# Kernel tuning notes

Hardware: AMD Instinct MI355X
Metric: run time of the kernel (lower is better)

The kernel has to match this reference:

```python
import jax, jax.numpy as jnp
import numpy as np

EPS = 1e-10        # matches eps in calculate_jeffreys_similarity
NEG = -1e30        # finite 'masked out' logit (avoids NaN for absent classes)
NORM_EPS = 1e-12   # F.normalize clamp


def setup_inputs() -> dict:
    key = jax.random.key(0)
    k1, k2, k3 = jax.random.split(key, 3)
    B, D, H, W = 4, 256, 256, 256
    C, P = 16, 5
    feature_map = jax.random.normal(k1, (B, D, H, W), dtype=jnp.float32)
    prototypes = jax.random.normal(k2, (C * P, D), dtype=jnp.float32)
    gt_mask = jax.random.randint(k3, (B, H, W), 0, C, dtype=jnp.int32)
    return {
        "feature_map": feature_map,
        "prototypes": prototypes,
        "gt_mask": gt_mask,
        "num_prototypes_per_class": P,
    }


def _loss(feature_map, prototypes, gt_mask, P):
    B, D, H, W = feature_map.shape
    N = H * W
    C = prototypes.shape[0] // P

    # [B, N, D] L2-normalized pixel features (F.normalize, eps=1e-12)
    feats = feature_map.reshape(B, D, N).transpose(0, 2, 1)
    feats = feats / jnp.maximum(jnp.linalg.norm(feats, axis=-1, keepdims=True), NORM_EPS)

    # [C, P, D] L2-normalized prototypes
    protos = prototypes.reshape(C, P, D)
    protos = protos / jnp.maximum(jnp.linalg.norm(protos, axis=-1, keepdims=True), NORM_EPS)

    # per-class pixel membership mask [B, C, N]
    mask = gt_mask.reshape(B, 1, N) == jnp.arange(C, dtype=gt_mask.dtype)[None, :, None]
    present = jnp.any(mask, axis=-1)                        # [B, C]

    # cosine similarities: [B, C, P, N]
    sims = jnp.einsum('bnd,cpd->bcpn', feats, protos)

    m = mask[:, :, None, :]                                 # [B, C, 1, N]
    # first softmax over the pixels of the class (original: softmax(similarities, dim=0))
    s1 = jax.nn.softmax(jnp.where(m, sims, NEG), axis=-1)
    # second softmax applied inside calculate_jeffreys_similarity (over the same gathered pixels)
    s2 = jax.nn.softmax(jnp.where(m, s1, NEG), axis=-1)

    # V = distribution + eps; off-mask positions are exactly eps, and since
    # eps*(log eps - log eps)=0 they contribute nothing to the KL sums below,
    # so summing over all N reproduces the gathered-pixel sum exactly.
    V = jnp.where(m, s2, 0.0) + EPS                          # [B, C, P, N]
    logV = jnp.log(V)

    A = jnp.sum(V * logV, axis=-1)                           # [B, C, P]
    # Bmat[b,c,i,j] = sum_n logV[i] * V[j]
    Bmat = jnp.einsum('bcin,bcjn->bcij', logV, V)
    # KL(V_j || V_i) = A[j] - Bmat[i, j]
    M = A[:, :, None, :] - Bmat                              # [B, C, P, P]
    J = M + jnp.swapaxes(M, -1, -2)                          # Jeffreys divergence (symmetric)
    simmat = jnp.exp(-J)                                     # pairwise similarity

    P_ = simmat.shape[-1]
    triu = jnp.triu(jnp.ones((P_, P_), dtype=simmat.dtype), k=1)
    num_pairs = P_ * (P_ - 1) // 2
    class_sim = jnp.sum(simmat * triu, axis=(-1, -2)) / num_pairs   # [B, C]

    # mean over classes that actually appear in the image; empty image -> 0
    class_sim = jnp.where(present, class_sim, 0.0)
    cnt = jnp.sum(present, axis=-1).astype(class_sim.dtype)          # [B]
    batch_loss = jnp.where(cnt > 0, jnp.sum(class_sim, axis=-1) / jnp.maximum(cnt, 1.0), 0.0)
    return jnp.sum(batch_loss) / B


def reference(feature_map, prototypes, gt_mask, num_prototypes_per_class):
    return _loss(feature_map, prototypes, gt_mask, num_prototypes_per_class)
```

## Files before the change

kernel.cpp:

```cpp
#include <hip/hip_runtime.h>
#include <math.h>

#define BB 4
#define DD 256
#define NN 65536
#define CC 16
#define PP 5
#define CP 80
#define EPSV 1e-10f
#define PITCH 264

#define OFF_PLANE  20480
#define OFF_ACC    (OFF_PLANE + BB * PP * NN)
#define ACC_FLOATS (320 + 320 + 64 + BB * CC * 16)

__device__ __forceinline__ unsigned short f2bf(float f) {
    unsigned int u = __float_as_uint(f);
    u += 0x7fffu + ((u >> 16) & 1u);
    return (unsigned short)(u >> 16);
}

__global__ void k_norm(const float* __restrict__ protos,
                       float* __restrict__ protosN,
                       float* __restrict__ acc) {
    if (blockIdx.x == CP) {
        for (int i = threadIdx.x; i < ACC_FLOATS; i += 256) acc[i] = 0.f;
        return;
    }
    int r = blockIdx.x;
    int d = threadIdx.x;
    float v = protos[r * DD + d];
    __shared__ float red[256];
    red[d] = v * v;
    __syncthreads();
    for (int s = 128; s > 0; s >>= 1) {
        if (d < s) red[d] += red[d + s];
        __syncthreads();
    }
    float inv = 1.f / fmaxf(sqrtf(red[0]), 1e-12f);
    protosN[r * DD + d] = v * inv;
}

__device__ __forceinline__ void loadgv(const float* __restrict__ fb, int g,
                                       float4 (&f)[8]) {
    const float* p = fb + (size_t)g * 8 * NN;
    #pragma unroll
    for (int k = 0; k < 8; ++k)
        f[k] = *reinterpret_cast<const float4*>(p + (size_t)k * NN);
}

__device__ __forceinline__ void compv(const char* lb0, const char* lb1,
                                      const char* lb2, const char* lb3,
                                      const float4 (&f)[8], int g,
                                      float (&dot)[4][PP], float (&nrm)[4]) {
    const char* lbs[4] = {lb0, lb1, lb2, lb3};
    #pragma unroll
    for (int x = 0; x < 4; ++x) {
        uint4 q[PP];
        #pragma unroll
        for (int p = 0; p < PP; ++p)
            q[p] = *reinterpret_cast<const uint4*>(lbs[x] + p * (PITCH * 2) + g * 16);
        #pragma unroll
        for (int k = 0; k < 8; ++k) {
            float fx = (&f[k].x)[x];
            nrm[x] = fmaf(fx, fx, nrm[x]);
            #pragma unroll
            for (int p = 0; p < PP; ++p) {
                unsigned int w = (&q[p].x)[k >> 1];
                float a = __uint_as_float((k & 1) ? (w & 0xffff0000u) : (w << 16));
                dot[x][p] = fmaf(fx, a, dot[x][p]);
            }
        }
    }
}

__global__ __launch_bounds__(256) void k_sims(const float* __restrict__ fmap,
                                              const float* __restrict__ protosN,
                                              const int* __restrict__ gt,
                                              float* __restrict__ plane,
                                              float* __restrict__ denom1,
                                              float* __restrict__ cnt) {
    __shared__ __align__(16) unsigned short lp[CP * PITCH];
    __shared__ float bins[CP];
    __shared__ float binc[CC];
    const int tid = threadIdx.x;
    const int b   = blockIdx.x >> 6;
    const int n0  = ((blockIdx.x & 63) << 10) + (tid << 2);

    if (tid < CP) bins[tid] = 0.f;
    if (tid < CC) binc[tid] = 0.f;

    for (int idx = tid; idx < 5120; idx += 256) {
        int cp = idx >> 6, q = idx & 63;
        float4 v = *reinterpret_cast<const float4*>(&protosN[(cp << 8) + (q << 2)]);
        unsigned int u0 = (unsigned int)f2bf(v.x) | ((unsigned int)f2bf(v.y) << 16);
        unsigned int u1 = (unsigned int)f2bf(v.z) | ((unsigned int)f2bf(v.w) << 16);
        *reinterpret_cast<uint2*>(reinterpret_cast<char*>(lp) + cp * (PITCH * 2) + (q << 3))
            = make_uint2(u0, u1);
    }
    __syncthreads();

    const int4 cls = *reinterpret_cast<const int4*>(&gt[(size_t)b * NN + n0]);
    const char* lpc = reinterpret_cast<const char*>(lp);
    const char* lb0 = lpc + cls.x * (PP * PITCH * 2);
    const char* lb1 = lpc + cls.y * (PP * PITCH * 2);
    const char* lb2 = lpc + cls.z * (PP * PITCH * 2);
    const char* lb3 = lpc + cls.w * (PP * PITCH * 2);
    const float* fb = fmap + (size_t)b * DD * NN + n0;

    float dot[4][PP] = {{0.f,0.f,0.f,0.f,0.f},{0.f,0.f,0.f,0.f,0.f},
                        {0.f,0.f,0.f,0.f,0.f},{0.f,0.f,0.f,0.f,0.f}};
    float nrm[4] = {0.f, 0.f, 0.f, 0.f};
    float4 fA[8], fB[8];

    loadgv(fb, 0, fA);
    #pragma unroll 1
    for (int g = 0; g < 32; g += 2) {
        loadgv(fb, g + 1, fB);
        compv(lb0, lb1, lb2, lb3, fA, g, dot, nrm);
        if (g < 30) loadgv(fb, g + 2, fA);
        compv(lb0, lb1, lb2, lb3, fB, g + 1, dot, nrm);
    }

    float inv[4];
    #pragma unroll
    for (int x = 0; x < 4; ++x) inv[x] = 1.f / fmaxf(sqrtf(nrm[x]), 1e-12f);

    const int c4[4] = {cls.x, cls.y, cls.z, cls.w};
    #pragma unroll
    for (int p = 0; p < PP; ++p) {
        float4 e;
        e.x = __expf(dot[0][p] * inv[0] - 1.f);
        e.y = __expf(dot[1][p] * inv[1] - 1.f);
        e.z = __expf(dot[2][p] * inv[2] - 1.f);
        e.w = __expf(dot[3][p] * inv[3] - 1.f);
        *reinterpret_cast<float4*>(&plane[(size_t)(b * PP + p) * NN + n0]) = e;
        atomicAdd(&bins[c4[0] * PP + p], e.x);
        atomicAdd(&bins[c4[1] * PP + p], e.y);
        atomicAdd(&bins[c4[2] * PP + p], e.z);
        atomicAdd(&bins[c4[3] * PP + p], e.w);
    }
    #pragma unroll
    for (int x = 0; x < 4; ++x) atomicAdd(&binc[c4[x]], 1.f);
    __syncthreads();
    if (tid < CP) atomicAdd(&denom1[b * CP + tid], bins[tid]);
    if (tid < CC) atomicAdd(&cnt[b * CC + tid], binc[tid]);
}

__global__ __launch_bounds__(256) void k_denom2(const int* __restrict__ gt,
                                                const float* __restrict__ plane,
                                                const float* __restrict__ denom1,
                                                float* __restrict__ denom2) {
    __shared__ float inv1s[CP];
    __shared__ float bins[4][CP];
    const int tid = threadIdx.x;
    const int w   = tid >> 6;
    const int b   = blockIdx.x >> 6;
    const int n0  = ((blockIdx.x & 63) << 10) + (tid << 2);
    if (tid < CP) inv1s[tid] = 1.f / denom1[b * CP + tid];
    for (int i = tid; i < 4 * CP; i += 256) (&bins[0][0])[i] = 0.f;
    __syncthreads();
    const int4 cls = *reinterpret_cast<const int4*>(&gt[(size_t)b * NN + n0]);
    #pragma unroll
    for (int p = 0; p < PP; ++p) {
        size_t idx = (size_t)(b * PP + p) * NN + n0;
        float4 e = *reinterpret_cast<const float4*>(&plane[idx]);
        atomicAdd(&bins[w][cls.x * PP + p], __expf(e.x * inv1s[cls.x * PP + p] - 1.f));
        atomicAdd(&bins[w][cls.y * PP + p], __expf(e.y * inv1s[cls.y * PP + p] - 1.f));
        atomicAdd(&bins[w][cls.z * PP + p], __expf(e.z * inv1s[cls.z * PP + p] - 1.f));
        atomicAdd(&bins[w][cls.w * PP + p], __expf(e.w * inv1s[cls.w * PP + p] - 1.f));
    }
    __syncthreads();
    if (tid < CP)
        atomicAdd(&denom2[b * CP + tid],
                  bins[0][tid] + bins[1][tid] + bins[2][tid] + bins[3][tid]);
}

__global__ __launch_bounds__(256) void k_bmat(const int* __restrict__ gt,
                                              const float* __restrict__ plane,
                                              const float* __restrict__ denom1,
                                              const float* __restrict__ denom2,
                                              float* __restrict__ Bbins) {
    __shared__ float inv1s[CP];
    __shared__ float inv2s[CP];
    __shared__ float sb[4][CC * 16];
    const int tid = threadIdx.x;
    const int w   = tid >> 6;
    const int b   = blockIdx.x >> 6;
    const int n0  = ((blockIdx.x & 63) << 10) + (tid << 2);
    if (tid < CP) {
        inv1s[tid] = 1.f / denom1[b * CP + tid];
        inv2s[tid] = 1.f / denom2[b * CP + tid];
    }
    for (int i = tid; i < 4 * CC * 16; i += 256) (&sb[0][0])[i] = 0.f;
    __syncthreads();
    const int4 cls = *reinterpret_cast<const int4*>(&gt[(size_t)b * NN + n0]);
    const int c4[4] = {cls.x, cls.y, cls.z, cls.w};
    float V[4][PP], L[4][PP];
    #pragma unroll
    for (int p = 0; p < PP; ++p) {
        size_t idx = (size_t)(b * PP + p) * NN + n0;
        float4 e = *reinterpret_cast<const float4*>(&plane[idx]);
        V[0][p] = fmaf(__expf(e.x * inv1s[cls.x * PP + p] - 1.f), inv2s[cls.x * PP + p], EPSV);
        V[1][p] = fmaf(__expf(e.y * inv1s[cls.y * PP + p] - 1.f), inv2s[cls.y * PP + p], EPSV);
        V[2][p] = fmaf(__expf(e.z * inv1s[cls.z * PP + p] - 1.f), inv2s[cls.z * PP + p], EPSV);
        V[3][p] = fmaf(__expf(e.w * inv1s[cls.w * PP + p] - 1.f), inv2s[cls.w * PP + p], EPSV);
    }
    #pragma unroll
    for (int q = 0; q < 4; ++q)
        #pragma unroll
        for (int p = 0; p < PP; ++p) L[q][p] = __logf(V[q][p]);
    #pragma unroll
    for (int q = 0; q < 4; ++q) {
        float* base = &sb[w][c4[q] * 16];
        #pragma unroll
        for (int i = 0; i < PP; ++i) atomicAdd(&base[i], L[q][i] * V[q][i]);
        int slot = 5;
        #pragma unroll
        for (int i = 0; i < PP; ++i)
            #pragma unroll
            for (int j = i + 1; j < PP; ++j) {
                atomicAdd(&base[slot], fmaf(L[q][i], V[q][j], L[q][j] * V[q][i]));
                ++slot;
            }
    }
    __syncthreads();
    for (int i = tid; i < CC * 16; i += 256)
        atomicAdd(&Bbins[b * CC * 16 + i], sb[0][i] + sb[1][i] + sb[2][i] + sb[3][i]);
}

__global__ void k_final(const float* __restrict__ Bbins,
                        const float* __restrict__ cnt,
                        float* __restrict__ out) {
    __shared__ float cs[BB * CC];
    __shared__ float pr[BB * CC];
    const int t = threadIdx.x;
    if (t < BB * CC) {
        const float* bb = &Bbins[t * 16];
        float s = 0.f;
        int slot = 5;
        #pragma unroll
        for (int i = 0; i < PP; ++i)
            for (int j = i + 1; j < PP; ++j) {
                float J = bb[i] + bb[j] - bb[slot];
                ++slot;
                s += __expf(-J);
            }
        bool present = cnt[t] > 0.f;
        cs[t] = present ? s * 0.1f : 0.f;
        pr[t] = present ? 1.f : 0.f;
    }
    __syncthreads();
    if (t == 0) {
        float total = 0.f;
        for (int b = 0; b < BB; ++b) {
            float sc = 0.f, np = 0.f;
            for (int c = 0; c < CC; ++c) { sc += cs[b * CC + c]; np += pr[b * CC + c]; }
            total += (np > 0.f) ? sc / np : 0.f;
        }
        out[0] = total / (float)BB;
    }
}

extern "C" void kernel_launch(void* const* d_in, const int* in_sizes, int n_in,
                              void* d_out, int out_size, void* d_ws, size_t ws_size,
                              hipStream_t stream) {
    const float* fmap   = (const float*)d_in[0];
    const float* protos = (const float*)d_in[1];
    const int*   gt     = (const int*)d_in[2];
    float* ws      = (float*)d_ws;
    float* protosN = ws;
    float* plane   = ws + OFF_PLANE;
    float* acc     = ws + OFF_ACC;
    float* denom1  = acc;
    float* denom2  = acc + 320;
    float* cnt     = acc + 640;
    float* Bbins   = acc + 704;
    float* out     = (float*)d_out;

    k_norm  <<<CP + 1, 256, 0, stream>>>(protos, protosN, acc);
    k_sims  <<<256, 256, 0, stream>>>(fmap, protosN, gt, plane, denom1, cnt);
    k_denom2<<<256, 256, 0, stream>>>(gt, plane, denom1, denom2);
    k_bmat  <<<256, 256, 0, stream>>>(gt, plane, denom1, denom2, Bbins);
    k_final <<<1, 64, 0, stream>>>(Bbins, cnt, out);
}
```

Before: 96.41 us.

## Fuse all stages into one cooperative kernel with grid syncs, keep sims in registers

Replaces the five separate launches with one cooperative kernel that separates the prototype normalisation, similarity, two softmax denominators, the Bmat accumulation and the final reduction with grid.sync. Per-pixel exp values now stay in registers across phases, so the plane buffer is no longer written to and re-read from global memory twice. It also swizzles the block-to-tile mapping, staggers each block's starting D chunk to spread memory traffic, and pads the shared bins to a stride of 17. In exchange it adds four grid-wide barriers and needs all 256 blocks to be co-resident.

```diff
diff --git a/kernel.cpp b/kernel.cpp
--- a/kernel.cpp
+++ b/kernel.cpp
@@ -1,5 +1,8 @@
 #include <hip/hip_runtime.h>
+#include <hip/hip_cooperative_groups.h>
 #include <math.h>
+
+namespace cg = cooperative_groups;
 
 #define BB 4
 #define DD 256
@@ -10,9 +13,8 @@
 #define EPSV 1e-10f
 #define PITCH 264
 
-#define OFF_PLANE  20480
-#define OFF_ACC    (OFF_PLANE + BB * PP * NN)
-#define ACC_FLOATS (320 + 320 + 64 + BB * CC * 16)
+#define OFF_ACC    20480
+#define ACC_FLOATS 1728
 
 __device__ __forceinline__ unsigned short f2bf(float f) {
     unsigned int u = __float_as_uint(f);
@@ -20,30 +22,9 @@
     return (unsigned short)(u >> 16);
 }
 
-__global__ void k_norm(const float* __restrict__ protos,
-                       float* __restrict__ protosN,
-                       float* __restrict__ acc) {
-    if (blockIdx.x == CP) {
-        for (int i = threadIdx.x; i < ACC_FLOATS; i += 256) acc[i] = 0.f;
-        return;
-    }
-    int r = blockIdx.x;
-    int d = threadIdx.x;
-    float v = protos[r * DD + d];
-    __shared__ float red[256];
-    red[d] = v * v;
-    __syncthreads();
-    for (int s = 128; s > 0; s >>= 1) {
-        if (d < s) red[d] += red[d + s];
-        __syncthreads();
-    }
-    float inv = 1.f / fmaxf(sqrtf(red[0]), 1e-12f);
-    protosN[r * DD + d] = v * inv;
-}
-
-__device__ __forceinline__ void loadgv(const float* __restrict__ fb, int g,
+__device__ __forceinline__ void loadgv(const float* __restrict__ fb, int gi,
                                        float4 (&f)[8]) {
-    const float* p = fb + (size_t)g * 8 * NN;
+    const float* p = fb + (size_t)gi * 8 * NN;
     #pragma unroll
     for (int k = 0; k < 8; ++k)
         f[k] = *reinterpret_cast<const float4*>(p + (size_t)k * NN);
@@ -51,7 +32,7 @@
 
 __device__ __forceinline__ void compv(const char* lb0, const char* lb1,
                                       const char* lb2, const char* lb3,
-                                      const float4 (&f)[8], int g,
+                                      const float4 (&f)[8], int gi,
                                       float (&dot)[4][PP], float (&nrm)[4]) {
     const char* lbs[4] = {lb0, lb1, lb2, lb3};
     #pragma unroll
@@ -59,7 +40,7 @@
         uint4 q[PP];
         #pragma unroll
         for (int p = 0; p < PP; ++p)
-            q[p] = *reinterpret_cast<const uint4*>(lbs[x] + p * (PITCH * 2) + g * 16);
+            q[p] = *reinterpret_cast<const uint4*>(lbs[x] + p * (PITCH * 2) + gi * 16);
         #pragma unroll
         for (int k = 0; k < 8; ++k) {
             float fx = (&f[k].x)[x];
@@ -74,33 +55,60 @@
     }
 }
 
-__global__ __launch_bounds__(256) void k_sims(const float* __restrict__ fmap,
-                                              const float* __restrict__ protosN,
-                                              const int* __restrict__ gt,
-                                              float* __restrict__ plane,
-                                              float* __restrict__ denom1,
-                                              float* __restrict__ cnt) {
-    __shared__ __align__(16) unsigned short lp[CP * PITCH];
-    __shared__ float bins[CP];
-    __shared__ float binc[CC];
+__global__ __launch_bounds__(256) void k_fused(const float* __restrict__ fmap,
+                                               const float* __restrict__ protos,
+                                               const int* __restrict__ gt,
+                                               float* __restrict__ protosN,
+                                               float* __restrict__ acc,
+                                               float* __restrict__ out) {
+    cg::grid_group grid = cg::this_grid();
+    __shared__ __align__(16) char smem[42624];
     const int tid = threadIdx.x;
-    const int b   = blockIdx.x >> 6;
-    const int n0  = ((blockIdx.x & 63) << 10) + (tid << 2);
+    const int bid = blockIdx.x;
+
+    float* denom1 = acc;
+    float* denom2 = acc + 320;
+    float* cnt    = acc + 640;
+    float* Bbins  = acc + 704;
+
+    if (bid < CP) {
+        float* red = reinterpret_cast<float*>(smem);
+        float v = protos[bid * DD + tid];
+        red[tid] = v * v;
+        __syncthreads();
+        for (int s = 128; s > 0; s >>= 1) {
+            if (tid < s) red[tid] += red[tid + s];
+            __syncthreads();
+        }
+        float inv = 1.f / fmaxf(sqrtf(red[0]), 1e-12f);
+        protosN[bid * DD + tid] = v * inv;
+    } else if (bid == CP) {
+        for (int i = tid; i < ACC_FLOATS; i += 256) acc[i] = 0.f;
+    }
+    grid.sync();
+
+    const int swz  = ((bid & 7) << 5) + (bid >> 3);
+    const int b    = swz >> 6;
+    const int n0   = ((swz & 63) << 10) + (tid << 2);
+    const int dph  = (bid & 7) << 2;
+
+    unsigned short* lp = reinterpret_cast<unsigned short*>(smem);
+    float* bins = reinterpret_cast<float*>(smem + 42240);
+    float* binc = reinterpret_cast<float*>(smem + 42560);
 
     if (tid < CP) bins[tid] = 0.f;
     if (tid < CC) binc[tid] = 0.f;
-
     for (int idx = tid; idx < 5120; idx += 256) {
         int cp = idx >> 6, q = idx & 63;
         float4 v = *reinterpret_cast<const float4*>(&protosN[(cp << 8) + (q << 2)]);
         unsigned int u0 = (unsigned int)f2bf(v.x) | ((unsigned int)f2bf(v.y) << 16);
         unsigned int u1 = (unsigned int)f2bf(v.z) | ((unsigned int)f2bf(v.w) << 16);
-        *reinterpret_cast<uint2*>(reinterpret_cast<char*>(lp) + cp * (PITCH * 2) + (q << 3))
-            = make_uint2(u0, u1);
+        *reinterpret_cast<uint2*>(smem + cp * (PITCH * 2) + (q << 3)) = make_uint2(u0, u1);
     }
     __syncthreads();
 
     const int4 cls = *reinterpret_cast<const int4*>(&gt[(size_t)b * NN + n0]);
+    const int c4[4] = {cls.x, cls.y, cls.z, cls.w};
     const char* lpc = reinterpret_cast<const char*>(lp);
     const char* lb0 = lpc + cls.x * (PP * PITCH * 2);
     const char* lb1 = lpc + cls.y * (PP * PITCH * 2);
@@ -113,152 +121,133 @@
     float nrm[4] = {0.f, 0.f, 0.f, 0.f};
     float4 fA[8], fB[8];
 
-    loadgv(fb, 0, fA);
+    loadgv(fb, dph, fA);
     #pragma unroll 1
     for (int g = 0; g < 32; g += 2) {
-        loadgv(fb, g + 1, fB);
-        compv(lb0, lb1, lb2, lb3, fA, g, dot, nrm);
-        if (g < 30) loadgv(fb, g + 2, fA);
-        compv(lb0, lb1, lb2, lb3, fB, g + 1, dot, nrm);
+        const int giA = (g + dph) & 31;
+        const int giB = (g + 1 + dph) & 31;
+        loadgv(fb, giB, fB);
+        compv(lb0, lb1, lb2, lb3, fA, giA, dot, nrm);
+        if (g < 30) loadgv(fb, (g + 2 + dph) & 31, fA);
+        compv(lb0, lb1, lb2, lb3, fB, giB, dot, nrm);
     }
 
     float inv[4];
     #pragma unroll
     for (int x = 0; x < 4; ++x) inv[x] = 1.f / fmaxf(sqrtf(nrm[x]), 1e-12f);
 
-    const int c4[4] = {cls.x, cls.y, cls.z, cls.w};
+    float u[4][PP];
     #pragma unroll
     for (int p = 0; p < PP; ++p) {
-        float4 e;
-        e.x = __expf(dot[0][p] * inv[0] - 1.f);
-        e.y = __expf(dot[1][p] * inv[1] - 1.f);
-        e.z = __expf(dot[2][p] * inv[2] - 1.f);
-        e.w = __expf(dot[3][p] * inv[3] - 1.f);
-        *reinterpret_cast<float4*>(&plane[(size_t)(b * PP + p) * NN + n0]) = e;
-        atomicAdd(&bins[c4[0] * PP + p], e.x);
-        atomicAdd(&bins[c4[1] * PP + p], e.y);
-        atomicAdd(&bins[c4[2] * PP + p], e.z);
-        atomicAdd(&bins[c4[3] * PP + p], e.w);
+        u[0][p] = __expf(dot[0][p] * inv[0] - 1.f);
+        u[1][p] = __expf(dot[1][p] * inv[1] - 1.f);
+        u[2][p] = __expf(dot[2][p] * inv[2] - 1.f);
+        u[3][p] = __expf(dot[3][p] * inv[3] - 1.f);
+        atomicAdd(&bins[c4[0] * PP + p], u[0][p]);
+        atomicAdd(&bins[c4[1] * PP + p], u[1][p]);
+        atomicAdd(&bins[c4[2] * PP + p], u[2][p]);
+        atomicAdd(&bins[c4[3] * PP + p], u[3][p]);
     }
     #pragma unroll
     for (int x = 0; x < 4; ++x) atomicAdd(&binc[c4[x]], 1.f);
     __syncthreads();
     if (tid < CP) atomicAdd(&denom1[b * CP + tid], bins[tid]);
     if (tid < CC) atomicAdd(&cnt[b * CC + tid], binc[tid]);
-}
-
-__global__ __launch_bounds__(256) void k_denom2(const int* __restrict__ gt,
-                                                const float* __restrict__ plane,
-                                                const float* __restrict__ denom1,
-                                                float* __restrict__ denom2) {
-    __shared__ float inv1s[CP];
-    __shared__ float bins[4][CP];
-    const int tid = threadIdx.x;
-    const int w   = tid >> 6;
-    const int b   = blockIdx.x >> 6;
-    const int n0  = ((blockIdx.x & 63) << 10) + (tid << 2);
-    if (tid < CP) inv1s[tid] = 1.f / denom1[b * CP + tid];
-    for (int i = tid; i < 4 * CP; i += 256) (&bins[0][0])[i] = 0.f;
-    __syncthreads();
-    const int4 cls = *reinterpret_cast<const int4*>(&gt[(size_t)b * NN + n0]);
-    #pragma unroll
-    for (int p = 0; p < PP; ++p) {
-        size_t idx = (size_t)(b * PP + p) * NN + n0;
-        float4 e = *reinterpret_cast<const float4*>(&plane[idx]);
-        atomicAdd(&bins[w][cls.x * PP + p], __expf(e.x * inv1s[cls.x * PP + p] - 1.f));
-        atomicAdd(&bins[w][cls.y * PP + p], __expf(e.y * inv1s[cls.y * PP + p] - 1.f));
-        atomicAdd(&bins[w][cls.z * PP + p], __expf(e.z * inv1s[cls.z * PP + p] - 1.f));
-        atomicAdd(&bins[w][cls.w * PP + p], __expf(e.w * inv1s[cls.w * PP + p] - 1.f));
-    }
-    __syncthreads();
-    if (tid < CP)
-        atomicAdd(&denom2[b * CP + tid],
-                  bins[0][tid] + bins[1][tid] + bins[2][tid] + bins[3][tid]);
-}
-
-__global__ __launch_bounds__(256) void k_bmat(const int* __restrict__ gt,
-                                              const float* __restrict__ plane,
-                                              const float* __restrict__ denom1,
-                                              const float* __restrict__ denom2,
-                                              float* __restrict__ Bbins) {
-    __shared__ float inv1s[CP];
-    __shared__ float inv2s[CP];
-    __shared__ float sb[4][CC * 16];
-    const int tid = threadIdx.x;
-    const int w   = tid >> 6;
-    const int b   = blockIdx.x >> 6;
-    const int n0  = ((blockIdx.x & 63) << 10) + (tid << 2);
-    if (tid < CP) {
-        inv1s[tid] = 1.f / denom1[b * CP + tid];
-        inv2s[tid] = 1.f / denom2[b * CP + tid];
-    }
-    for (int i = tid; i < 4 * CC * 16; i += 256) (&sb[0][0])[i] = 0.f;
-    __syncthreads();
-    const int4 cls = *reinterpret_cast<const int4*>(&gt[(size_t)b * NN + n0]);
-    const int c4[4] = {cls.x, cls.y, cls.z, cls.w};
-    float V[4][PP], L[4][PP];
-    #pragma unroll
-    for (int p = 0; p < PP; ++p) {
-        size_t idx = (size_t)(b * PP + p) * NN + n0;
-        float4 e = *reinterpret_cast<const float4*>(&plane[idx]);
-        V[0][p] = fmaf(__expf(e.x * inv1s[cls.x * PP + p] - 1.f), inv2s[cls.x * PP + p], EPSV);
-        V[1][p] = fmaf(__expf(e.y * inv1s[cls.y * PP + p] - 1.f), inv2s[cls.y * PP + p], EPSV);
-        V[2][p] = fmaf(__expf(e.z * inv1s[cls.z * PP + p] - 1.f), inv2s[cls.z * PP + p], EPSV);
-        V[3][p] = fmaf(__expf(e.w * inv1s[cls.w * PP + p] - 1.f), inv2s[cls.w * PP + p], EPSV);
-    }
-    #pragma unroll
-    for (int q = 0; q < 4; ++q)
-        #pragma unroll
-        for (int p = 0; p < PP; ++p) L[q][p] = __logf(V[q][p]);
-    #pragma unroll
-    for (int q = 0; q < 4; ++q) {
-        float* base = &sb[w][c4[q] * 16];
-        #pragma unroll
-        for (int i = 0; i < PP; ++i) atomicAdd(&base[i], L[q][i] * V[q][i]);
-        int slot = 5;
-        #pragma unroll
-        for (int i = 0; i < PP; ++i)
-            #pragma unroll
-            for (int j = i + 1; j < PP; ++j) {
-                atomicAdd(&base[slot], fmaf(L[q][i], V[q][j], L[q][j] * V[q][i]));
-                ++slot;
+    grid.sync();
+
+    {
+        float* inv1s = reinterpret_cast<float*>(smem);
+        float* wbins = reinterpret_cast<float*>(smem + 320);
+        if (tid < CP) inv1s[tid] = 1.f / denom1[b * CP + tid];
+        for (int i = tid; i < 4 * CP; i += 256) wbins[i] = 0.f;
+        __syncthreads();
+        const int w = tid >> 6;
+        #pragma unroll
+        for (int p = 0; p < PP; ++p) {
+            u[0][p] = __expf(u[0][p] * inv1s[c4[0] * PP + p] - 1.f);
+            u[1][p] = __expf(u[1][p] * inv1s[c4[1] * PP + p] - 1.f);
+            u[2][p] = __expf(u[2][p] * inv1s[c4[2] * PP + p] - 1.f);
+            u[3][p] = __expf(u[3][p] * inv1s[c4[3] * PP + p] - 1.f);
+            atomicAdd(&wbins[w * CP + c4[0] * PP + p], u[0][p]);
+            atomicAdd(&wbins[w * CP + c4[1] * PP + p], u[1][p]);
+            atomicAdd(&wbins[w * CP + c4[2] * PP + p], u[2][p]);
+            atomicAdd(&wbins[w * CP + c4[3] * PP + p], u[3][p]);
+        }
+        __syncthreads();
+        if (tid < CP)
+            atomicAdd(&denom2[b * CP + tid],
+                      wbins[tid] + wbins[80 + tid] + wbins[160 + tid] + wbins[240 + tid]);
+    }
+    grid.sync();
+
+    {
+        float* inv2s = reinterpret_cast<float*>(smem);
+        float* sb    = reinterpret_cast<float*>(smem + 320);
+        if (tid < CP) inv2s[tid] = 1.f / denom2[b * CP + tid];
+        for (int i = tid; i < 4 * 272; i += 256) sb[i] = 0.f;
+        __syncthreads();
+        const int w = tid >> 6;
+        float V[4][PP], L[4][PP];
+        #pragma unroll
+        for (int q = 0; q < 4; ++q) {
+            #pragma unroll
+            for (int p = 0; p < PP; ++p) {
+                V[q][p] = fmaf(u[q][p], inv2s[c4[q] * PP + p], EPSV);
+                L[q][p] = __logf(V[q][p]);
             }
-    }
-    __syncthreads();
-    for (int i = tid; i < CC * 16; i += 256)
-        atomicAdd(&Bbins[b * CC * 16 + i], sb[0][i] + sb[1][i] + sb[2][i] + sb[3][i]);
-}
-
-__global__ void k_final(const float* __restrict__ Bbins,
-                        const float* __restrict__ cnt,
-                        float* __restrict__ out) {
-    __shared__ float cs[BB * CC];
-    __shared__ float pr[BB * CC];
-    const int t = threadIdx.x;
-    if (t < BB * CC) {
-        const float* bb = &Bbins[t * 16];
-        float s = 0.f;
-        int slot = 5;
-        #pragma unroll
-        for (int i = 0; i < PP; ++i)
-            for (int j = i + 1; j < PP; ++j) {
-                float J = bb[i] + bb[j] - bb[slot];
-                ++slot;
-                s += __expf(-J);
+        }
+        #pragma unroll
+        for (int q = 0; q < 4; ++q) {
+            float* base = &sb[w * 272 + c4[q] * 17];
+            #pragma unroll
+            for (int i = 0; i < PP; ++i) atomicAdd(&base[i], L[q][i] * V[q][i]);
+            int slot = 5;
+            #pragma unroll
+            for (int i = 0; i < PP; ++i)
+                #pragma unroll
+                for (int j = i + 1; j < PP; ++j) {
+                    atomicAdd(&base[slot], fmaf(L[q][i], V[q][j], L[q][j] * V[q][i]));
+                    ++slot;
+                }
+        }
+        __syncthreads();
+        {
+            int c = tid >> 4, s = tid & 15;
+            float t = sb[c * 17 + s] + sb[272 + c * 17 + s]
+                    + sb[544 + c * 17 + s] + sb[816 + c * 17 + s];
+            atomicAdd(&Bbins[b * 256 + tid], t);
+        }
+    }
+    grid.sync();
+
+    if (bid == 0) {
+        float* cs = reinterpret_cast<float*>(smem);
+        float* pr = reinterpret_cast<float*>(smem + 256);
+        if (tid < BB * CC) {
+            const float* bb = &Bbins[tid * 16];
+            float s = 0.f;
+            int slot = 5;
+            #pragma unroll
+            for (int i = 0; i < PP; ++i)
+                for (int j = i + 1; j < PP; ++j) {
+                    float J = bb[i] + bb[j] - bb[slot];
+                    ++slot;
+                    s += __expf(-J);
+                }
+            bool present = cnt[tid] > 0.f;
+            cs[tid] = present ? s * 0.1f : 0.f;
+            pr[tid] = present ? 1.f : 0.f;
+        }
+        __syncthreads();
+        if (tid == 0) {
+            float total = 0.f;
+            for (int bb2 = 0; bb2 < BB; ++bb2) {
+                float sc = 0.f, np = 0.f;
+                for (int c = 0; c < CC; ++c) { sc += cs[bb2 * CC + c]; np += pr[bb2 * CC + c]; }
+                total += (np > 0.f) ? sc / np : 0.f;
             }
-        bool present = cnt[t] > 0.f;
-        cs[t] = present ? s * 0.1f : 0.f;
-        pr[t] = present ? 1.f : 0.f;
-    }
-    __syncthreads();
-    if (t == 0) {
-        float total = 0.f;
-        for (int b = 0; b < BB; ++b) {
-            float sc = 0.f, np = 0.f;
-            for (int c = 0; c < CC; ++c) { sc += cs[b * CC + c]; np += pr[b * CC + c]; }
-            total += (np > 0.f) ? sc / np : 0.f;
-        }
-        out[0] = total / (float)BB;
+            out[0] = total / (float)BB;
+        }
     }
 }
 
@@ -270,17 +259,11 @@
     const int*   gt     = (const int*)d_in[2];
     float* ws      = (float*)d_ws;
     float* protosN = ws;
-    float* plane   = ws + OFF_PLANE;
     float* acc     = ws + OFF_ACC;
-    float* denom1  = acc;
-    float* denom2  = acc + 320;
-    float* cnt     = acc + 640;
-    float* Bbins   = acc + 704;
     float* out     = (float*)d_out;
 
-    k_norm  <<<CP + 1, 256, 0, stream>>>(protos, protosN, acc);
-    k_sims  <<<256, 256, 0, stream>>>(fmap, protosN, gt, plane, denom1, cnt);
-    k_denom2<<<256, 256, 0, stream>>>(gt, plane, denom1, denom2);
-    k_bmat  <<<256, 256, 0, stream>>>(gt, plane, denom1, denom2, Bbins);
-    k_final <<<1, 64, 0, stream>>>(Bbins, cnt, out);
-}
+    void* args[6] = {(void*)&fmap, (void*)&protos, (void*)&gt,
+                     (void*)&protosN, (void*)&acc, (void*)&out};
+    hipLaunchCooperativeKernel(reinterpret_cast<void*>(k_fused),
+                               dim3(256), dim3(256), args, 0, stream);
+}
```

New measurement: 199.1 us. 107% more time.
